# Optimization experiments

Measured on AMD Instinct MI355X. Metric: run time of the kernel, lower is better.

The kernel has to match this reference:

```python
import jax, jax.numpy as jnp
import numpy as np

EMBED = 768
HEADS = 12
FACTOR = 2
LN_EPS = 1e-5


def layer_norm(x, gamma, beta):
    mu = jnp.mean(x, axis=-1, keepdims=True)
    var = jnp.mean(jnp.square(x - mu), axis=-1, keepdims=True)
    return (x - mu) * jax.lax.rsqrt(var + LN_EPS) * gamma + beta


def setup_inputs() -> dict:
    key = jax.random.key(0)
    ks = jax.random.split(key, 8)
    B, S, E = 8, 1024, EMBED
    H = FACTOR * E
    s_e = 1.0 / np.sqrt(E)
    s_h = 1.0 / np.sqrt(H)
    return {
        "x": jax.random.normal(ks[0], (B, S, E), jnp.float32),
        "Wq": jax.random.normal(ks[1], (E, E), jnp.float32) * s_e,
        "Wk": jax.random.normal(ks[2], (E, E), jnp.float32) * s_e,
        "Wv": jax.random.normal(ks[3], (E, E), jnp.float32) * s_e,
        "W1": jax.random.normal(ks[4], (E, H), jnp.float32) * s_e,
        "b1": jnp.zeros((H,), jnp.float32),
        "W2": jax.random.normal(ks[5], (H, E), jnp.float32) * s_h,
        "b2": jnp.zeros((E,), jnp.float32),
        "g1": jnp.ones((E,), jnp.float32),
        "beta1": jnp.zeros((E,), jnp.float32),
        "g2": jnp.ones((E,), jnp.float32),
        "beta2": jnp.zeros((E,), jnp.float32),
    }


def reference(x, Wq, Wk, Wv, W1, b1, W2, b2, g1, beta1, g2, beta2):
    B, S, E = x.shape
    hd = E // HEADS
    # NOTE: original reshapes (B,S,E)->(B,H,S,hd) WITHOUT transposing heads
    # (non-standard: mixes sequence blocks across heads) - replicated faithfully.
    q = (x @ Wq).reshape(B, HEADS, S, hd)
    k = (x @ Wk).reshape(B, HEADS, S, hd)
    v = (x @ Wv).reshape(B, HEADS, S, hd)
    # no 1/sqrt(d) scaling in the original
    attn = jax.nn.softmax(jnp.einsum('bnqd,bnkd->bnqk', q, k), axis=-1)
    # NOTE: original einsum 'bnqk,bnvd->bnqd' sums over BOTH k and v
    # (value is sum-pooled over its sequence axis) - replicated faithfully.
    out = jnp.einsum('bnqk,bnvd->bnqd', attn, v)
    out = out.transpose(0, 2, 1, 3).reshape(B, S, E)
    a = x + layer_norm(out, g1, beta1)
    # GELU after BOTH linears (exact GELU, torch default)
    h = jax.nn.gelu(a @ W1 + b1, approximate=False)
    m = jax.nn.gelu(h @ W2 + b2, approximate=False)
    return x + layer_norm(m, g2, beta2)
```

## Files before the change

### kernel.cpp

```cpp
#include <hip/hip_runtime.h>
#include <hip/hip_bf16.h>
#include <math.h>

#define E_ 768
#define HID_ 1536
#define SQ_ 1024

typedef unsigned short u16;
using bf16x8 = __attribute__((ext_vector_type(8))) __bf16;
using f32x4  = __attribute__((ext_vector_type(4))) float;

__device__ __forceinline__ u16 f2bf(float f) {
  union { float f; unsigned u; } v; v.f = f;
  unsigned r = v.u + 0x7FFFu + ((v.u >> 16) & 1u);
  return (u16)(r >> 16);
}

__device__ __forceinline__ float gelu_f(float x) {
  return 0.5f * x * (1.0f + erff(x * 0.70710678118654752f));
}

#define GLDS16(gp, sp) __builtin_amdgcn_global_load_lds( \
    (__attribute__((address_space(1))) const void*)(const void*)(gp), \
    (__attribute__((address_space(3))) void*)(void*)(sp), 16, 0, 0)

__global__ void prep_kernel(const float* __restrict__ x, const float* __restrict__ W1,
                            const float* __restrict__ W2, u16* __restrict__ xb,
                            u16* __restrict__ W1T, u16* __restrict__ W2T) {
  __shared__ float T[64 * 65];
  int bid = blockIdx.x, t = threadIdx.x;
  if (bid < 6144) {
    int base = bid * 1024 + t * 4;
    const float4 v = *reinterpret_cast<const float4*>(x + base);
    ushort4 o; o.x = f2bf(v.x); o.y = f2bf(v.y); o.z = f2bf(v.z); o.w = f2bf(v.w);
    *reinterpret_cast<ushort4*>(xb + base) = o;
    return;
  }
  const float* in; u16* out; int R_in, C_in, rt, ct;
  if (bid < 6432) {
    int b2 = bid - 6144; in = W1; out = W1T; R_in = 768; C_in = 1536;
    rt = b2 / 24; ct = b2 % 24;
  } else {
    int b3 = bid - 6432; in = W2; out = W2T; R_in = 1536; C_in = 768;
    rt = b3 / 12; ct = b3 % 12;
  }
  int r0 = rt << 6, c0 = ct << 6;
  int tr = t >> 4, tc4 = (t & 15) << 2;
#pragma unroll
  for (int i = 0; i < 4; ++i) {
    int row = tr + (i << 4);
    const float4 v = *reinterpret_cast<const float4*>(in + (size_t)(r0 + row) * C_in + c0 + tc4);
    T[row * 65 + tc4 + 0] = v.x;
    T[row * 65 + tc4 + 1] = v.y;
    T[row * 65 + tc4 + 2] = v.z;
    T[row * 65 + tc4 + 3] = v.w;
  }
  __syncthreads();
#pragma unroll
  for (int i = 0; i < 4; ++i) {
    int orow = tr + (i << 4);
    ushort4 o;
    o.x = f2bf(T[(tc4 + 0) * 65 + orow]);
    o.y = f2bf(T[(tc4 + 1) * 65 + orow]);
    o.z = f2bf(T[(tc4 + 2) * 65 + orow]);
    o.w = f2bf(T[(tc4 + 3) * 65 + orow]);
    *reinterpret_cast<ushort4*>(out + (size_t)(c0 + orow) * R_in + r0 + tc4) = o;
  }
}

__global__ void rowsum_kernel(const float* __restrict__ x, float* __restrict__ Rp) {
  int bid = blockIdx.x;
  int r = bid >> 2, c = bid & 3;
  int b = r / 12, n = r % 12;
  int t = threadIdx.x;
  int u0 = n << 10;
  int s_lo = u0 / 12;
  int s_hi = (u0 + 1023) / 12;
  int cnt = s_hi - s_lo + 1;
  int cs = s_lo + (cnt * c) / 4;
  int ce = s_lo + (cnt * (c + 1)) / 4;
  float acc[12][3];
#pragma unroll
  for (int g = 0; g < 12; ++g)
    for (int q = 0; q < 3; ++q) acc[g][q] = 0.f;
  const float* xp = x + (size_t)b * SQ_ * E_;
  for (int s = cs; s < ce; ++s) {
    float v0 = xp[(size_t)s * E_ + t];
    float v1 = xp[(size_t)s * E_ + t + 256];
    float v2 = xp[(size_t)s * E_ + t + 512];
    int du = 12 * s - u0;
#pragma unroll
    for (int g = 0; g < 12; ++g) {
      int u = du + g;
      if (u >= 0 && u < 1024) { acc[g][0] += v0; acc[g][1] += v1; acc[g][2] += v2; }
    }
  }
  float* Rr = Rp + (size_t)bid * 9216;
#pragma unroll
  for (int g = 0; g < 12; ++g) {
    Rr[g * 768 + t]       = acc[g][0];
    Rr[g * 768 + t + 256] = acc[g][1];
    Rr[g * 768 + t + 512] = acc[g][2];
  }
}

__global__ void ygemm_kernel(const float* __restrict__ Rp, const float* __restrict__ Wv,
                             float* __restrict__ P2) {
  int g = blockIdx.x, r = blockIdx.y;
  int t = threadIdx.x;
  int d = t & 63, sub = t >> 6;
  const float* R0 = Rp + (size_t)r * 4 * 9216 + g * 768;
  const float* wp = Wv + g * 64 + d;
  float acc = 0.f;
  int j0 = sub * 192;
#pragma unroll 4
  for (int jj = 0; jj < 192; ++jj) {
    int j = j0 + jj;
    float rv = R0[j] + R0[9216 + j] + R0[2 * 9216 + j] + R0[3 * 9216 + j];
    acc += rv * wp[(size_t)j * 768];
  }
  __shared__ float red[256];
  red[t] = acc;
  __syncthreads();
  if (sub == 0)
    P2[((size_t)r * 12 + g) * 64 + d] = red[d] + red[64 + d] + red[128 + d] + red[192 + d];
}

__global__ void ln1_kernel(const float* __restrict__ P2, const float* __restrict__ g1,
                           const float* __restrict__ be1, float* __restrict__ L1) {
  int b = blockIdx.x, t = threadIdx.x;
  float y[3];
#pragma unroll
  for (int q = 0; q < 3; ++q) {
    int e = t + (q << 8);
    int n = e >> 6, d = e & 63;
    const float* Pp = P2 + ((size_t)(b * 12 + n) * 12) * 64 + d;
    float s = 0.f;
#pragma unroll
    for (int g = 0; g < 12; ++g) s += Pp[g << 6];
    y[q] = s;
  }
  float s = y[0] + y[1] + y[2];
  float sq = y[0] * y[0] + y[1] * y[1] + y[2] * y[2];
  __shared__ float red[8];
#pragma unroll
  for (int o = 32; o > 0; o >>= 1) { s += __shfl_down(s, o, 64); sq += __shfl_down(sq, o, 64); }
  if ((t & 63) == 0) { red[(t >> 6) * 2] = s; red[(t >> 6) * 2 + 1] = sq; }
  __syncthreads();
  s  = red[0] + red[2] + red[4] + red[6];
  sq = red[1] + red[3] + red[5] + red[7];
  float mu = s * (1.f / 768.f);
  float var = sq * (1.f / 768.f) - mu * mu;
  float rs = rsqrtf(var + 1e-5f);
#pragma unroll
  for (int q = 0; q < 3; ++q) {
    int e = t + (q << 8);
    L1[b * 768 + e] = (y[q] - mu) * rs * g1[e] + be1[e];
  }
}

__global__ void c1_kernel(const float* __restrict__ L1, const float* __restrict__ W1,
                          const float* __restrict__ b1, float* __restrict__ C1) {
  int bid = blockIdx.x;
  int b = bid / 48, c = bid % 48;
  int t = threadIdx.x;
  __shared__ float Ls[768];
  __shared__ float red[8][32];
  for (int q = t; q < 768; q += 256) Ls[q] = L1[b * 768 + q];
  __syncthreads();
  int tc = t & 31, ts = t >> 5;
  int n = c * 32 + tc;
  float acc = 0.f;
  int j0 = ts * 96;
#pragma unroll 4
  for (int j = j0; j < j0 + 96; ++j) acc += Ls[j] * W1[(size_t)j * HID_ + n];
  red[ts][tc] = acc;
  __syncthreads();
  if (ts == 0) {
    float s = b1[n];
#pragma unroll
    for (int k = 0; k < 8; ++k) s += red[k][tc];
    C1[b * HID_ + n] = s;
  }
}

template <int OUT_KIND>
__global__ __launch_bounds__(256, 2) void gemm_bt_kernel(
    const u16* __restrict__ A, const u16* __restrict__ BT,
    const float* __restrict__ bias, void* __restrict__ Cout,
    int M, int N, int K) {
  __shared__ __align__(16) u16 As[128 * 64];
  __shared__ __align__(16) u16 Bs[128 * 64];
  int t = threadIdx.x;
  int lane = t & 63, w = t >> 6;
  int bm = blockIdx.y << 7, bn = blockIdx.x << 7;
  int wm = (w >> 1) << 6, wn = (w & 1) << 6;
  int quad = lane >> 4, l16 = lane & 15;
  f32x4 acc[4][4] = {};

  for (int k0 = 0; k0 < K; k0 += 64) {
    __syncthreads();
#pragma unroll
    for (int i = 0; i < 4; ++i) {
      int ci = t + (i << 8);
      int r = ci >> 3, csw = ci & 7;
      int kc = csw ^ (r & 7);
      const u16* ga = A + (size_t)(bm + r) * K + k0 + (kc << 3);
      GLDS16(ga, As + ci * 8);
      const u16* gb = BT + (size_t)(bn + r) * K + k0 + (kc << 3);
      GLDS16(gb, Bs + ci * 8);
    }
    __builtin_amdgcn_s_waitcnt(0);
    __syncthreads();
#pragma unroll
    for (int ks = 0; ks < 2; ++ks) {
      bf16x8 af[4], bf[4];
      int kc = (ks << 2) + quad;
#pragma unroll
      for (int mt = 0; mt < 4; ++mt) {
        int row = wm + (mt << 4) + l16;
        af[mt] = *reinterpret_cast<const bf16x8*>(As + row * 64 + ((kc ^ (row & 7)) << 3));
      }
#pragma unroll
      for (int nt = 0; nt < 4; ++nt) {
        int row = wn + (nt << 4) + l16;
        bf[nt] = *reinterpret_cast<const bf16x8*>(Bs + row * 64 + ((kc ^ (row & 7)) << 3));
      }
#pragma unroll
      for (int mt = 0; mt < 4; ++mt)
#pragma unroll
        for (int nt = 0; nt < 4; ++nt)
          acc[mt][nt] = __builtin_amdgcn_mfma_f32_16x16x32_bf16(af[mt], bf[nt], acc[mt][nt], 0, 0, 0);
    }
  }

#pragma unroll
  for (int mt = 0; mt < 4; ++mt) {
    int row0 = bm + wm + (mt << 4) + (quad << 2);
#pragma unroll
    for (int nt = 0; nt < 4; ++nt) {
      int col = bn + wn + (nt << 4) + l16;
      float bv = (OUT_KIND == 0) ? bias[(bm >> 10) * N + col] : bias[col];
#pragma unroll
      for (int rr = 0; rr < 4; ++rr) {
        float v = gelu_f(acc[mt][nt][rr] + bv);
        size_t idx = (size_t)(row0 + rr) * N + col;
        if (OUT_KIND == 0) ((u16*)Cout)[idx] = f2bf(v);
        else               ((float*)Cout)[idx] = v;
      }
    }
  }
}

__global__ void ln2_kernel(const float* __restrict__ m, const float* __restrict__ x,
                           const float* __restrict__ g2, const float* __restrict__ be2,
                           float* __restrict__ out) {
  int row = blockIdx.x, t = threadIdx.x;
  const float* mr = m + (size_t)row * 768;
  float v0 = mr[t], v1 = mr[t + 256], v2 = mr[t + 512];
  float s = v0 + v1 + v2;
  float sq = v0 * v0 + v1 * v1 + v2 * v2;
  __shared__ float red[8];
#pragma unroll
  for (int o = 32; o > 0; o >>= 1) { s += __shfl_down(s, o, 64); sq += __shfl_down(sq, o, 64); }
  if ((t & 63) == 0) { red[(t >> 6) * 2] = s; red[(t >> 6) * 2 + 1] = sq; }
  __syncthreads();
  s  = red[0] + red[2] + red[4] + red[6];
  sq = red[1] + red[3] + red[5] + red[7];
  float mu = s * (1.f / 768.f);
  float var = sq * (1.f / 768.f) - mu * mu;
  float rs = rsqrtf(var + 1e-5f);
  const float* xr = x + (size_t)row * 768;
  float* orow = out + (size_t)row * 768;
  orow[t]       = xr[t]       + (v0 - mu) * rs * g2[t]       + be2[t];
  orow[t + 256] = xr[t + 256] + (v1 - mu) * rs * g2[t + 256] + be2[t + 256];
  orow[t + 512] = xr[t + 512] + (v2 - mu) * rs * g2[t + 512] + be2[t + 512];
}

extern "C" void kernel_launch(void* const* d_in, const int* in_sizes, int n_in,
                              void* d_out, int out_size, void* d_ws, size_t ws_size,
                              hipStream_t stream) {
  const float* x   = (const float*)d_in[0];
  const float* Wv  = (const float*)d_in[3];
  const float* W1  = (const float*)d_in[4];
  const float* b1  = (const float*)d_in[5];
  const float* W2  = (const float*)d_in[6];
  const float* b2  = (const float*)d_in[7];
  const float* g1  = (const float*)d_in[8];
  const float* be1 = (const float*)d_in[9];
  const float* g2  = (const float*)d_in[10];
  const float* be2 = (const float*)d_in[11];
  float* out = (float*)d_out;

  char* ws = (char*)d_ws;
  u16*   xb  = (u16*)(ws);
  u16*   W1T = (u16*)(ws + 12582912);
  u16*   W2T = (u16*)(ws + 14942208);
  u16*   h   = (u16*)(ws + 17301504);
  float* Rp  = (float*)(ws + 17301504);
  float* P2  = (float*)(ws + 42467328);
  float* L1  = (float*)(ws + 42762240);
  float* C1  = (float*)(ws + 42786816);
  float* mm  = out;

  prep_kernel<<<6720, 256, 0, stream>>>(x, W1, W2, xb, W1T, W2T);
  rowsum_kernel<<<384, 256, 0, stream>>>(x, Rp);
  ygemm_kernel<<<dim3(12, 96), 256, 0, stream>>>(Rp, Wv, P2);
  ln1_kernel<<<8, 256, 0, stream>>>(P2, g1, be1, L1);
  c1_kernel<<<384, 256, 0, stream>>>(L1, W1, b1, C1);
  gemm_bt_kernel<0><<<dim3(12, 64), 256, 0, stream>>>(xb, W1T, C1, (void*)h, 8192, 1536, 768);
  gemm_bt_kernel<1><<<dim3(6, 64), 256, 0, stream>>>(h, W2T, b2, (void*)mm, 8192, 768, 1536);
  ln2_kernel<<<8192, 256, 0, stream>>>(mm, x, g2, be2, out);
}
```

Before: 257.3 us.

## Split-K second GEMM, XCD-aware block mapping, bf16 rowsum input, defer GELU to LN2

The second GEMM is split into two K-halves so it launches 768 blocks instead of 384. One half writes fp32 partials to the output buffer and the other writes bf16 partials into the reused xb buffer. Bias, GELU and the sum of the partials move into the LN2 kernel. Both GEMMs use a 1D grid that maps blocks so each XCD works on a contiguous M range, for better L2 locality. Rowsum now reads the bf16 copy of x, halving its traffic at some precision cost, and ygemm gets four independent accumulators. The risks are extra partial-sum traffic and bf16 rounding of one partial.

```diff
diff --git a/kernel.cpp b/kernel.cpp
--- a/kernel.cpp
+++ b/kernel.cpp
@@ -15,7 +15,9 @@
   unsigned r = v.u + 0x7FFFu + ((v.u >> 16) & 1u);
   return (u16)(r >> 16);
 }
-
+__device__ __forceinline__ float bf2f(u16 h) {
+  union { unsigned u; float f; } v; v.u = ((unsigned)h) << 16; return v.f;
+}
 __device__ __forceinline__ float gelu_f(float x) {
   return 0.5f * x * (1.0f + erff(x * 0.70710678118654752f));
 }
@@ -68,7 +70,7 @@
   }
 }
 
-__global__ void rowsum_kernel(const float* __restrict__ x, float* __restrict__ Rp) {
+__global__ void rowsum_kernel(const u16* __restrict__ xb, float* __restrict__ Rp) {
   int bid = blockIdx.x;
   int r = bid >> 2, c = bid & 3;
   int b = r / 12, n = r % 12;
@@ -83,11 +85,11 @@
 #pragma unroll
   for (int g = 0; g < 12; ++g)
     for (int q = 0; q < 3; ++q) acc[g][q] = 0.f;
-  const float* xp = x + (size_t)b * SQ_ * E_;
+  const u16* xp = xb + (size_t)b * SQ_ * E_;
   for (int s = cs; s < ce; ++s) {
-    float v0 = xp[(size_t)s * E_ + t];
-    float v1 = xp[(size_t)s * E_ + t + 256];
-    float v2 = xp[(size_t)s * E_ + t + 512];
+    float v0 = bf2f(xp[(size_t)s * E_ + t]);
+    float v1 = bf2f(xp[(size_t)s * E_ + t + 256]);
+    float v2 = bf2f(xp[(size_t)s * E_ + t + 512]);
     int du = 12 * s - u0;
 #pragma unroll
     for (int g = 0; g < 12; ++g) {
@@ -111,16 +113,22 @@
   int d = t & 63, sub = t >> 6;
   const float* R0 = Rp + (size_t)r * 4 * 9216 + g * 768;
   const float* wp = Wv + g * 64 + d;
-  float acc = 0.f;
+  float a0 = 0.f, a1 = 0.f, a2 = 0.f, a3 = 0.f;
   int j0 = sub * 192;
-#pragma unroll 4
-  for (int jj = 0; jj < 192; ++jj) {
+#pragma unroll 2
+  for (int jj = 0; jj < 192; jj += 4) {
     int j = j0 + jj;
-    float rv = R0[j] + R0[9216 + j] + R0[2 * 9216 + j] + R0[3 * 9216 + j];
-    acc += rv * wp[(size_t)j * 768];
+    float r0v = R0[j + 0] + R0[9216 + j + 0] + R0[18432 + j + 0] + R0[27648 + j + 0];
+    float r1v = R0[j + 1] + R0[9216 + j + 1] + R0[18432 + j + 1] + R0[27648 + j + 1];
+    float r2v = R0[j + 2] + R0[9216 + j + 2] + R0[18432 + j + 2] + R0[27648 + j + 2];
+    float r3v = R0[j + 3] + R0[9216 + j + 3] + R0[18432 + j + 3] + R0[27648 + j + 3];
+    a0 += r0v * wp[(size_t)(j + 0) * 768];
+    a1 += r1v * wp[(size_t)(j + 1) * 768];
+    a2 += r2v * wp[(size_t)(j + 2) * 768];
+    a3 += r3v * wp[(size_t)(j + 3) * 768];
   }
   __shared__ float red[256];
-  red[t] = acc;
+  red[t] = (a0 + a1) + (a2 + a3);
   __syncthreads();
   if (sub == 0)
     P2[((size_t)r * 12 + g) * 64 + d] = red[d] + red[64 + d] + red[128 + d] + red[192 + d];
@@ -184,30 +192,36 @@
   }
 }
 
-template <int OUT_KIND>
+template <int MODE>
 __global__ __launch_bounds__(256, 2) void gemm_bt_kernel(
     const u16* __restrict__ A, const u16* __restrict__ BT,
-    const float* __restrict__ bias, void* __restrict__ Cout,
-    int M, int N, int K) {
+    const float* __restrict__ bias, void* __restrict__ out0, void* __restrict__ out1,
+    int N, int lda, int ldb) {
   __shared__ __align__(16) u16 As[128 * 64];
   __shared__ __align__(16) u16 Bs[128 * 64];
+  int bid = blockIdx.x;
+  int xcd = bid & 7, idx = bid >> 3;
+  int mloc, n_, k_off, kk = 0;
+  if (MODE == 0) { mloc = idx / 12; n_ = idx % 12; k_off = 0; }
+  else           { kk = idx / 48; int rem = idx % 48; mloc = rem / 6; n_ = rem % 6; k_off = kk * 768; }
+  int bm = (xcd * 8 + mloc) << 7, bn = n_ << 7;
+
   int t = threadIdx.x;
   int lane = t & 63, w = t >> 6;
-  int bm = blockIdx.y << 7, bn = blockIdx.x << 7;
   int wm = (w >> 1) << 6, wn = (w & 1) << 6;
   int quad = lane >> 4, l16 = lane & 15;
   f32x4 acc[4][4] = {};
 
-  for (int k0 = 0; k0 < K; k0 += 64) {
+  for (int k0 = 0; k0 < 768; k0 += 64) {
     __syncthreads();
 #pragma unroll
     for (int i = 0; i < 4; ++i) {
       int ci = t + (i << 8);
       int r = ci >> 3, csw = ci & 7;
       int kc = csw ^ (r & 7);
-      const u16* ga = A + (size_t)(bm + r) * K + k0 + (kc << 3);
+      const u16* ga = A + (size_t)(bm + r) * lda + k_off + k0 + (kc << 3);
       GLDS16(ga, As + ci * 8);
-      const u16* gb = BT + (size_t)(bn + r) * K + k0 + (kc << 3);
+      const u16* gb = BT + (size_t)(bn + r) * ldb + k_off + k0 + (kc << 3);
       GLDS16(gb, Bs + ci * 8);
     }
     __builtin_amdgcn_s_waitcnt(0);
@@ -240,24 +254,29 @@
 #pragma unroll
     for (int nt = 0; nt < 4; ++nt) {
       int col = bn + wn + (nt << 4) + l16;
-      float bv = (OUT_KIND == 0) ? bias[(bm >> 10) * N + col] : bias[col];
+      float bv = (MODE == 0) ? bias[(bm >> 10) * N + col] : 0.f;
 #pragma unroll
       for (int rr = 0; rr < 4; ++rr) {
-        float v = gelu_f(acc[mt][nt][rr] + bv);
-        size_t idx = (size_t)(row0 + rr) * N + col;
-        if (OUT_KIND == 0) ((u16*)Cout)[idx] = f2bf(v);
-        else               ((float*)Cout)[idx] = v;
+        float v = acc[mt][nt][rr] + bv;
+        size_t idxo = (size_t)(row0 + rr) * N + col;
+        if (MODE == 0)       ((u16*)out0)[idxo] = f2bf(gelu_f(v));
+        else if (kk == 0)    ((float*)out0)[idxo] = v;
+        else                 ((u16*)out1)[idxo] = f2bf(v);
       }
     }
   }
 }
 
-__global__ void ln2_kernel(const float* __restrict__ m, const float* __restrict__ x,
+__global__ void ln2_kernel(const float* __restrict__ p0, const u16* __restrict__ p1,
+                           const float* __restrict__ x, const float* __restrict__ b2,
                            const float* __restrict__ g2, const float* __restrict__ be2,
                            float* __restrict__ out) {
   int row = blockIdx.x, t = threadIdx.x;
-  const float* mr = m + (size_t)row * 768;
-  float v0 = mr[t], v1 = mr[t + 256], v2 = mr[t + 512];
+  const float* pr = p0 + (size_t)row * 768;
+  const u16* qr = p1 + (size_t)row * 768;
+  float v0 = gelu_f(pr[t]       + bf2f(qr[t])       + b2[t]);
+  float v1 = gelu_f(pr[t + 256] + bf2f(qr[t + 256]) + b2[t + 256]);
+  float v2 = gelu_f(pr[t + 512] + bf2f(qr[t + 512]) + b2[t + 512]);
   float s = v0 + v1 + v2;
   float sq = v0 * v0 + v1 * v1 + v2 * v2;
   __shared__ float red[8];
@@ -301,14 +320,14 @@
   float* P2  = (float*)(ws + 42467328);
   float* L1  = (float*)(ws + 42762240);
   float* C1  = (float*)(ws + 42786816);
-  float* mm  = out;
+  u16*   p1  = xb;
 
   prep_kernel<<<6720, 256, 0, stream>>>(x, W1, W2, xb, W1T, W2T);
-  rowsum_kernel<<<384, 256, 0, stream>>>(x, Rp);
+  rowsum_kernel<<<384, 256, 0, stream>>>(xb, Rp);
   ygemm_kernel<<<dim3(12, 96), 256, 0, stream>>>(Rp, Wv, P2);
   ln1_kernel<<<8, 256, 0, stream>>>(P2, g1, be1, L1);
   c1_kernel<<<384, 256, 0, stream>>>(L1, W1, b1, C1);
-  gemm_bt_kernel<0><<<dim3(12, 64), 256, 0, stream>>>(xb, W1T, C1, (void*)h, 8192, 1536, 768);
-  gemm_bt_kernel<1><<<dim3(6, 64), 256, 0, stream>>>(h, W2T, b2, (void*)mm, 8192, 768, 1536);
-  ln2_kernel<<<8192, 256, 0, stream>>>(mm, x, g2, be2, out);
-}
+  gemm_bt_kernel<0><<<768, 256, 0, stream>>>(xb, W1T, C1, (void*)h, nullptr, 1536, 768, 768);
+  gemm_bt_kernel<1><<<768, 256, 0, stream>>>(h, W2T, nullptr, (void*)out, (void*)p1, 768, 1536, 1536);
+  ln2_kernel<<<8192, 256, 0, stream>>>(out, p1, x, b2, g2, be2, out);
+}
```

Result: faster. 242.0 us (-5.9%).
